# Kernel optimization log

Hardware: AMD Instinct MI355X
Metric: run time of the kernel (lower is better)

## Reference

```python
import jax, jax.numpy as jnp
import numpy as np

COUPLING = 0.12
EPS = 1e-08
EMBED_DIM = 16
H = 4
REL_MAX_DIST = 64
PAST_LEN = 524288


def setup_inputs() -> dict:
    key = jax.random.key(0)
    ks = jax.random.split(key, 7)
    return {
        "candidate": jax.random.normal(ks[0], (EMBED_DIM, 2), dtype=jnp.float32),
        "z_past": jax.random.normal(ks[1], (PAST_LEN, EMBED_DIM, 2), dtype=jnp.float32),
        "heads_w": jax.random.normal(ks[2], (H, 2 * EMBED_DIM, 4 * EMBED_DIM), dtype=jnp.float32) * 0.05,
        "heads_b": jax.random.normal(ks[3], (H, 2 * EMBED_DIM), dtype=jnp.float32) * 0.05,
        "out_w": jax.random.normal(ks[4], (2 * EMBED_DIM, H * 2 * EMBED_DIM), dtype=jnp.float32) * 0.05,
        "out_b": jax.random.normal(ks[5], (2 * EMBED_DIM,), dtype=jnp.float32) * 0.05,
        "rel_bias": jax.random.normal(ks[6], (2 * REL_MAX_DIST + 1, 2), dtype=jnp.float32) * 0.02,
        "norm_scale": jnp.ones((1,), dtype=jnp.float32),
        "pos": PAST_LEN,
    }


def reference(candidate, z_past, heads_w, heads_b, out_w, out_b, rel_bias, norm_scale, pos):
    # candidate: [D,2] (real/imag), z_past: [P,D,2]
    P, D = z_past.shape[0], z_past.shape[1]
    # features_c = cat([z_curr_rep, z_past], -1); view_as_real + flatten -> [P, 4D]
    feats = jnp.concatenate(
        [jnp.broadcast_to(candidate[None], (P, D, 2)), z_past], axis=1
    ).reshape(P, 4 * D)
    # 4 small MLP heads, tanh, concat: [P, H, 2D] -> mean over past -> [H*2D]
    h = jnp.tanh(jnp.einsum("pd,hod->pho", feats, heads_w) + heads_b[None])
    combined_mean = h.reshape(P, -1).mean(axis=0)
    out = out_w @ combined_mean + out_b          # [2D]
    mod = out.reshape(D, 2)                      # complex mod as real/imag pair
    # relative positional bias: mean over gathered (clipped) indices
    rel = jnp.arange(pos - P, pos)
    idx = jnp.clip(rel + REL_MAX_DIST, 0, 2 * REL_MAX_DIST)
    bias_mean = rel_bias[idx].mean(axis=0)       # [2]
    # z_new = candidate + COUPLING * (mod + bias_mean)
    z = candidate + COUPLING * (mod + bias_mean[None, :])
    # tanh applied independently to real and imag parts
    z = jnp.tanh(z)
    max_int = jnp.max(jnp.sum(z * z, axis=-1))   # max |z|^2
    scale = norm_scale[0] / jnp.sqrt(max_int + EPS)
    return jnp.where(max_int > 0, z * scale, z)  # [D,2]
```

## Files before the change

### kernel.cpp

```cpp
#include <hip/hip_runtime.h>
#include <hip/hip_bf16.h>
#include <math.h>

#define COUPLING 0.12f
#define EPSV 1e-8f
#define SCALE2L2E 2.8853900817779268f

typedef __attribute__((ext_vector_type(8))) short bf16x8;
typedef __attribute__((ext_vector_type(4))) float f32x4;

__device__ __forceinline__ float tanh_from_e2(float y) {
    float e = __builtin_amdgcn_exp2f(y);
    float r = __builtin_amdgcn_rcpf(1.0f + e);
    return fmaf(-2.0f, r, 1.0f);
}
__device__ __forceinline__ float tanh_fast(float x) {
    return tanh_from_e2(SCALE2L2E * x);
}
__device__ __forceinline__ float sig_e2(float y) {
    float e = __builtin_amdgcn_exp2f(y);
    return __builtin_amdgcn_rcpf(1.0f + e);
}

__device__ __forceinline__ short f2bf(float f) {
    __hip_bfloat16 h = __float2bfloat16(f);
    return __builtin_bit_cast(short, h);
}

__global__ __launch_bounds__(256, 4) void phot_main(
    const float* __restrict__ z_past,
    const float* __restrict__ heads_w,
    const float* __restrict__ heads_b,
    const float* __restrict__ cand,
    float* __restrict__ partials,
    int P, int NB)
{
    __shared__ float wacc[128];
    __shared__ float cpre_l[128];
    __shared__ __align__(16) unsigned short wbf_l[128][32];
    __shared__ __align__(16) unsigned short zb[3][4][512];

    const int tid  = threadIdx.x;
    const int lane = tid & 63;
    const int wv   = tid >> 6;
    const int col  = lane & 15;
    const int kg   = lane >> 4;

    if (tid < 128) {
        const float* wr = heads_w + (size_t)tid * 64;
        float s0 = heads_b[tid], s1 = 0.f, s2 = 0.f, s3 = 0.f;
        #pragma unroll
        for (int k = 0; k < 32; k += 4) {
            s0 = fmaf(wr[k+0], cand[k+0], s0);
            s1 = fmaf(wr[k+1], cand[k+1], s1);
            s2 = fmaf(wr[k+2], cand[k+2], s2);
            s3 = fmaf(wr[k+3], cand[k+3], s3);
        }
        cpre_l[tid] = SCALE2L2E * ((s0 + s1) + (s2 + s3));
        #pragma unroll
        for (int k = 0; k < 32; ++k)
            wbf_l[tid][k] = (unsigned short)f2bf(SCALE2L2E * wr[32 + k]);
    }
    __syncthreads();

    const int g0 = wv * 2, g1 = g0 + 1;
    const bf16x8 bfA = *(const bf16x8*)&wbf_l[g0 * 16 + col][kg * 8];
    const bf16x8 bfB = *(const bf16x8*)&wbf_l[g1 * 16 + col][kg * 8];
    const float  cpA = cpre_l[g0 * 16 + col];
    const float  cpB = cpre_l[g1 * 16 + col];

    f32x4 accA = {0,0,0,0}, accB = {0,0,0,0};

    const int T  = (P + 15) >> 4;
    const int Tf = P >> 4;
    const int b  = blockIdx.x;
    const int K  = (b < T) ? ((T - 1 - b) / NB + 1) : 0;
    const int PH = (K + 3) >> 2;

    const int sr = lane >> 2;
    const int sc = lane & 3;
    const int woff = sr * 32 + ((sc ^ (sr & 3)) << 3);

    const int roff = col * 32 + ((kg ^ (col & 3)) << 3);

    f32x4 preA, preB;

    #define SLOADP(ph) { \
        const int j_ = 4 * (ph) + wv; \
        if (j_ < K) { \
            const int tt_ = b + j_ * NB; \
            int grow = tt_ * 16 + sr; if (grow > P - 1) grow = P - 1; \
            const float* g_ = z_past + (size_t)grow * 32 + sc * 8; \
            preA = *(const f32x4*)g_; \
            preB = *(const f32x4*)(g_ + 4); \
        } }
    #define SWRITEP(ph) { \
        const int j_ = 4 * (ph) + wv; \
        if (j_ < K) { \
            bf16x8 w_; \
            w_[0]=f2bf(preA[0]); w_[1]=f2bf(preA[1]); w_[2]=f2bf(preA[2]); w_[3]=f2bf(preA[3]); \
            w_[4]=f2bf(preB[0]); w_[5]=f2bf(preB[1]); w_[6]=f2bf(preB[2]); w_[7]=f2bf(preB[3]); \
            *(bf16x8*)(&zb[(ph) % 3][wv][woff]) = w_; \
        } }
    #define CTILE(p, j) { \
        const int jj_ = 4 * (p) + (j); \
        if (jj_ < K) { \
            const int tt_ = b + jj_ * NB; \
            const bf16x8 a_ = *(const bf16x8*)(&zb[(p) % 3][j][roff]); \
            const int base_ = tt_ * 16; \
            if (base_ + 16 <= P) { \
                f32x4 c_ = {cpA, cpA, cpA, cpA}; \
                f32x4 d_ = __builtin_amdgcn_mfma_f32_16x16x32_bf16(a_, bfA, c_, 0, 0, 0); \
                accA[0] += sig_e2(d_[0]); accA[1] += sig_e2(d_[1]); \
                accA[2] += sig_e2(d_[2]); accA[3] += sig_e2(d_[3]); \
                c_ = {cpB, cpB, cpB, cpB}; \
                d_ = __builtin_amdgcn_mfma_f32_16x16x32_bf16(a_, bfB, c_, 0, 0, 0); \
                accB[0] += sig_e2(d_[0]); accB[1] += sig_e2(d_[1]); \
                accB[2] += sig_e2(d_[2]); accB[3] += sig_e2(d_[3]); \
            } else { \
                const int r0_ = base_ + kg * 4; \
                f32x4 c_ = {cpA, cpA, cpA, cpA}; \
                f32x4 d_ = __builtin_amdgcn_mfma_f32_16x16x32_bf16(a_, bfA, c_, 0, 0, 0); \
                if (r0_ + 0 < P) accA[0] += sig_e2(d_[0]); \
                if (r0_ + 1 < P) accA[1] += sig_e2(d_[1]); \
                if (r0_ + 2 < P) accA[2] += sig_e2(d_[2]); \
                if (r0_ + 3 < P) accA[3] += sig_e2(d_[3]); \
                c_ = {cpB, cpB, cpB, cpB}; \
                d_ = __builtin_amdgcn_mfma_f32_16x16x32_bf16(a_, bfB, c_, 0, 0, 0); \
                if (r0_ + 0 < P) accB[0] += sig_e2(d_[0]); \
                if (r0_ + 1 < P) accB[1] += sig_e2(d_[1]); \
                if (r0_ + 2 < P) accB[2] += sig_e2(d_[2]); \
                if (r0_ + 3 < P) accB[3] += sig_e2(d_[3]); \
            } \
        } }

    #define SYNC { asm volatile("s_waitcnt lgkmcnt(0)" ::: "memory"); \
                   __builtin_amdgcn_s_barrier(); }

    if (K > 0) {
        SLOADP(0)
        SWRITEP(0)
        SLOADP(1)
        SYNC

        for (int p = 0; p < PH; ++p) {
            if (p + 1 < PH) SWRITEP(p + 1);
            if (p + 2 < PH) SLOADP(p + 2);
            CTILE(p, 0) CTILE(p, 1) CTILE(p, 2) CTILE(p, 3)
            SYNC
        }
    }
    #undef SLOADP
    #undef SWRITEP
    #undef CTILE
    #undef SYNC

    float nsum = 0.0f;
    if (K > 0) {
        int nfull = (b < Tf) ? ((Tf - 1 - b) / NB + 1) : 0;
        nsum = 4.0f * (float)nfull;
        if (Tf < T && b <= Tf && ((Tf - b) % NB) == 0) {
            int prem = P - Tf * 16;
            int nv = prem - kg * 4; if (nv < 0) nv = 0; if (nv > 4) nv = 4;
            nsum += (float)nv;
        }
    }

    float sA = nsum - 2.0f * ((accA[0] + accA[1]) + (accA[2] + accA[3]));
    sA += __shfl_xor(sA, 16, 64);
    sA += __shfl_xor(sA, 32, 64);
    float sB = nsum - 2.0f * ((accB[0] + accB[1]) + (accB[2] + accB[3]));
    sB += __shfl_xor(sB, 16, 64);
    sB += __shfl_xor(sB, 32, 64);
    if (lane < 16) {
        wacc[g0 * 16 + lane] = sA;
        wacc[g1 * 16 + lane] = sB;
    }
    __syncthreads();
    if (tid < 128) {
        partials[(size_t)b * 128 + tid] = wacc[tid];
    }
}

__global__ __launch_bounds__(1024) void phot_finalize(
    const float* __restrict__ partials, int nblk, int P,
    const float* __restrict__ out_w,
    const float* __restrict__ out_b,
    const float* __restrict__ rel_bias,
    const float* __restrict__ cand,
    const float* __restrict__ norm_scale,
    const int* __restrict__ posp,
    float* __restrict__ out)
{
    __shared__ __align__(16) float sh[4096];
    __shared__ float  cm[128];
    __shared__ float  outv[32];
    __shared__ double db[512];
    __shared__ float  bm[2];

    const int t   = threadIdx.x;
    const int chg = t & 31;
    const int sl  = t >> 5;

    const int cnt = nblk >> 5;
    const float* p0 = partials + (size_t)(sl * cnt) * 128 + chg * 4;
    f32x4 a0 = {0,0,0,0}, a1 = {0,0,0,0}, a2 = {0,0,0,0}, a3 = {0,0,0,0};
    int i = 0;
    for (; i + 4 <= cnt; i += 4) {
        a0 += *(const f32x4*)(p0 + (size_t)(i+0) * 128);
        a1 += *(const f32x4*)(p0 + (size_t)(i+1) * 128);
        a2 += *(const f32x4*)(p0 + (size_t)(i+2) * 128);
        a3 += *(const f32x4*)(p0 + (size_t)(i+3) * 128);
    }
    for (; i < cnt; ++i) a0 += *(const f32x4*)(p0 + (size_t)i * 128);
    f32x4 acc = (a0 + a1) + (a2 + a3);
    *(f32x4*)&sh[sl * 128 + chg * 4] = acc;
    __syncthreads();

    if (t < 128) {
        float s = 0.0f;
        #pragma unroll
        for (int s2 = 0; s2 < 32; ++s2) s += sh[t + 128 * s2];
        cm[t] = s / (float)P;
    }

    if (t < 512) {
        const int c = t >> 8, j = t & 255;
        double v = 0.0;
        if (j <= 128) {
            const long long pos = (long long)(*posp);
            const long long a = pos - (long long)P + 64;
            double cnt2;
            if (j == 0) {
                long long hi = -a; if (hi > (long long)P - 1) hi = (long long)P - 1;
                cnt2 = (hi >= 0) ? (double)(hi + 1) : 0.0;
            } else if (j == 128) {
                long long lo = 128 - a; if (lo < 0) lo = 0;
                cnt2 = (lo <= (long long)P - 1) ? (double)((long long)P - lo) : 0.0;
            } else {
                long long p = (long long)j - a;
                cnt2 = (p >= 0 && p < (long long)P) ? 1.0 : 0.0;
            }
            v = cnt2 * (double)rel_bias[2*j + c];
        }
        db[t] = v;
    }
    __syncthreads();
    #pragma unroll
    for (int s = 128; s >= 1; s >>= 1) {
        if (t < 512 && (t & 255) < s) db[t] += db[t + s];
        __syncthreads();
    }
    if (t < 2) bm[t] = (float)(db[t << 8] / (double)P);
    __syncthreads();

    if (t < 32) {
        const float* wr = out_w + t * 128;
        float o0 = out_b[t], o1 = 0.f, o2 = 0.f, o3 = 0.f;
        #pragma unroll
        for (int j = 0; j < 128; j += 4) {
            o0 = fmaf(wr[j+0], cm[j+0], o0);
            o1 = fmaf(wr[j+1], cm[j+1], o1);
            o2 = fmaf(wr[j+2], cm[j+2], o2);
            o3 = fmaf(wr[j+3], cm[j+3], o3);
        }
        outv[t] = (o0+o1) + (o2+o3);
    }
    __syncthreads();

    if (t < 32) {
        float zt = tanh_fast(cand[t] + COUPLING * (outv[t] + bm[t & 1]));
        float other = __shfl_xor(zt, 1, 64);
        float m = fmaf(zt, zt, other * other);
        #pragma unroll
        for (int off = 2; off < 32; off <<= 1) m = fmaxf(m, __shfl_xor(m, off, 64));
        float scale = norm_scale[0] / sqrtf(m + EPSV);
        out[t] = (m > 0.0f) ? zt * scale : zt;
    }
}

extern "C" void kernel_launch(void* const* d_in, const int* in_sizes, int n_in,
                              void* d_out, int out_size, void* d_ws, size_t ws_size,
                              hipStream_t stream)
{
    const float* cand       = (const float*)d_in[0];
    const float* z_past     = (const float*)d_in[1];
    const float* heads_w    = (const float*)d_in[2];
    const float* heads_b    = (const float*)d_in[3];
    const float* out_w      = (const float*)d_in[4];
    const float* out_b      = (const float*)d_in[5];
    const float* rel_bias   = (const float*)d_in[6];
    const float* norm_scale = (const float*)d_in[7];
    const int*   posp       = (const int*)d_in[8];

    const int P = in_sizes[1] / 32;

    int nblk = 1024;
    size_t need = (size_t)nblk * 128 * sizeof(float);
    if (need > ws_size) {
        nblk = (int)(ws_size / (128 * sizeof(float)));
        nblk &= ~31;
        if (nblk < 32) nblk = 32;
    }
    float* partials = (float*)d_ws;

    phot_main<<<nblk, 256, 0, stream>>>(z_past, heads_w, heads_b, cand,
                                        partials, P, nblk);
    phot_finalize<<<1, 1024, 0, stream>>>(partials, nblk, P, out_w, out_b,
                                          rel_bias, cand, norm_scale, posp,
                                          (float*)d_out);
}
```

Before: 37.63 us.

## Double-buffer staging registers to keep global loads in flight across compute

The main streaming loop is unrolled by two and uses two sets of staging registers. The global load for the next-but-one phase is issued before the MFMA/sigmoid work on the current phase, and the bf16 conversion and LDS write for the next phase are moved after that compute. This keeps more loads in flight and hides HBM latency behind compute. A sched_barrier after each block barrier stops the compiler from moving instructions across it. The reduce kernel also gets a special path for 32 partials per slice that issues 16 vector loads at once to raise memory parallelism, at the cost of more VGPRs.

```diff
diff --git a/kernel.cpp b/kernel.cpp
--- a/kernel.cpp
+++ b/kernel.cpp
@@ -83,23 +83,25 @@
 
     const int roff = col * 32 + ((kg ^ (col & 3)) << 3);
 
-    f32x4 preA, preB;
-
-    #define SLOADP(ph) { \
+    f32x4 preA0, preB0, preA1, preB1;
+
+    #define SLOADP(ph, S) { \
         const int j_ = 4 * (ph) + wv; \
         if (j_ < K) { \
             const int tt_ = b + j_ * NB; \
             int grow = tt_ * 16 + sr; if (grow > P - 1) grow = P - 1; \
             const float* g_ = z_past + (size_t)grow * 32 + sc * 8; \
-            preA = *(const f32x4*)g_; \
-            preB = *(const f32x4*)(g_ + 4); \
+            preA##S = *(const f32x4*)g_; \
+            preB##S = *(const f32x4*)(g_ + 4); \
         } }
-    #define SWRITEP(ph) { \
+    #define SWRITEP(ph, S) { \
         const int j_ = 4 * (ph) + wv; \
         if (j_ < K) { \
             bf16x8 w_; \
-            w_[0]=f2bf(preA[0]); w_[1]=f2bf(preA[1]); w_[2]=f2bf(preA[2]); w_[3]=f2bf(preA[3]); \
-            w_[4]=f2bf(preB[0]); w_[5]=f2bf(preB[1]); w_[6]=f2bf(preB[2]); w_[7]=f2bf(preB[3]); \
+            w_[0]=f2bf(preA##S[0]); w_[1]=f2bf(preA##S[1]); \
+            w_[2]=f2bf(preA##S[2]); w_[3]=f2bf(preA##S[3]); \
+            w_[4]=f2bf(preB##S[0]); w_[5]=f2bf(preB##S[1]); \
+            w_[6]=f2bf(preB##S[2]); w_[7]=f2bf(preB##S[3]); \
             *(bf16x8*)(&zb[(ph) % 3][wv][woff]) = w_; \
         } }
     #define CTILE(p, j) { \
@@ -135,19 +137,28 @@
         } }
 
     #define SYNC { asm volatile("s_waitcnt lgkmcnt(0)" ::: "memory"); \
-                   __builtin_amdgcn_s_barrier(); }
+                   __builtin_amdgcn_s_barrier(); \
+                   __builtin_amdgcn_sched_barrier(0); }
 
     if (K > 0) {
-        SLOADP(0)
-        SWRITEP(0)
-        SLOADP(1)
+        SLOADP(0, 0)
+        SWRITEP(0, 0)
+        SLOADP(1, 1)
         SYNC
 
-        for (int p = 0; p < PH; ++p) {
-            if (p + 1 < PH) SWRITEP(p + 1);
-            if (p + 2 < PH) SLOADP(p + 2);
-            CTILE(p, 0) CTILE(p, 1) CTILE(p, 2) CTILE(p, 3)
-            SYNC
+        for (int p = 0; p < PH; p += 2) {
+            {
+                SLOADP(p + 2, 0)
+                CTILE(p, 0) CTILE(p, 1) CTILE(p, 2) CTILE(p, 3)
+                SWRITEP(p + 1, 1)
+                SYNC
+            }
+            {
+                SLOADP(p + 3, 1)
+                CTILE(p + 1, 0) CTILE(p + 1, 1) CTILE(p + 1, 2) CTILE(p + 1, 3)
+                SWRITEP(p + 2, 0)
+                SYNC
+            }
         }
     }
     #undef SLOADP
@@ -204,16 +215,35 @@
 
     const int cnt = nblk >> 5;
     const float* p0 = partials + (size_t)(sl * cnt) * 128 + chg * 4;
-    f32x4 a0 = {0,0,0,0}, a1 = {0,0,0,0}, a2 = {0,0,0,0}, a3 = {0,0,0,0};
-    int i = 0;
-    for (; i + 4 <= cnt; i += 4) {
-        a0 += *(const f32x4*)(p0 + (size_t)(i+0) * 128);
-        a1 += *(const f32x4*)(p0 + (size_t)(i+1) * 128);
-        a2 += *(const f32x4*)(p0 + (size_t)(i+2) * 128);
-        a3 += *(const f32x4*)(p0 + (size_t)(i+3) * 128);
-    }
-    for (; i < cnt; ++i) a0 += *(const f32x4*)(p0 + (size_t)i * 128);
-    f32x4 acc = (a0 + a1) + (a2 + a3);
+    f32x4 acc = {0,0,0,0};
+    if (cnt == 32) {
+        f32x4 v[16];
+        #pragma unroll
+        for (int i = 0; i < 16; ++i) v[i] = *(const f32x4*)(p0 + (size_t)i * 128);
+        f32x4 s0 = {0,0,0,0}, s1 = {0,0,0,0}, s2 = {0,0,0,0}, s3 = {0,0,0,0};
+        #pragma unroll
+        for (int i = 0; i < 16; i += 4) {
+            s0 += v[i+0]; s1 += v[i+1]; s2 += v[i+2]; s3 += v[i+3];
+        }
+        #pragma unroll
+        for (int i = 0; i < 16; ++i) v[i] = *(const f32x4*)(p0 + (size_t)(16 + i) * 128);
+        #pragma unroll
+        for (int i = 0; i < 16; i += 4) {
+            s0 += v[i+0]; s1 += v[i+1]; s2 += v[i+2]; s3 += v[i+3];
+        }
+        acc = (s0 + s1) + (s2 + s3);
+    } else {
+        f32x4 a0 = {0,0,0,0}, a1 = {0,0,0,0}, a2 = {0,0,0,0}, a3 = {0,0,0,0};
+        int i = 0;
+        for (; i + 4 <= cnt; i += 4) {
+            a0 += *(const f32x4*)(p0 + (size_t)(i+0) * 128);
+            a1 += *(const f32x4*)(p0 + (size_t)(i+1) * 128);
+            a2 += *(const f32x4*)(p0 + (size_t)(i+2) * 128);
+            a3 += *(const f32x4*)(p0 + (size_t)(i+3) * 128);
+        }
+        for (; i < cnt; ++i) a0 += *(const f32x4*)(p0 + (size_t)i * 128);
+        acc = (a0 + a1) + (a2 + a3);
+    }
     *(f32x4*)&sh[sl * 128 + chg * 4] = acc;
     __syncthreads();
 
```

Result: faster. 36.40 us (-3.3%).
